# Kernel tuning notes

Hardware: AMD Instinct MI355X
Metric: run time of the kernel (lower is better)

## Reference

```python
import jax, jax.numpy as jnp
import numpy as np

N_ENT = 100000
N_REL = 500
IN_DIM = 128
OUT_DIM = 128
N_TRIP = 250000
BN_EPS = 1e-5
LRELU_SLOPE = 0.01


def setup_inputs() -> dict:
    key = jax.random.key(0)
    ks = jax.random.split(key, 10)
    heads = jax.random.randint(ks[0], (N_TRIP, 1), 0, N_ENT, dtype=jnp.int32)
    tails = jax.random.randint(ks[1], (N_TRIP, 1), 0, N_ENT, dtype=jnp.int32)
    rels = jax.random.randint(ks[2], (N_TRIP, 1), 0, N_REL, dtype=jnp.int32)
    triplets = jnp.concatenate([heads, tails, rels], axis=1)
    embed_range = (6.0 + 2.0) / OUT_DIM  # (margin + epsilon) / out_dim
    ent_embed = jax.random.uniform(ks[3], (N_ENT, IN_DIM), jnp.float32, -embed_range, embed_range)
    rel_embed = jax.random.uniform(ks[4], (N_REL, IN_DIM), jnp.float32, -embed_range, embed_range)
    a_w = jax.random.normal(ks[5], (OUT_DIM, 3 * IN_DIM), jnp.float32) * (1.414 * (2.0 / (3 * IN_DIM + OUT_DIM)) ** 0.5)
    a_b = jnp.zeros((OUT_DIM,), jnp.float32)
    a2_w = jax.random.normal(ks[6], (1, OUT_DIM), jnp.float32) * (1.414 * (2.0 / (OUT_DIM + 1)) ** 0.5)
    a2_b = jnp.zeros((1,), jnp.float32)
    return dict(
        triplets=triplets,
        ent_embed=ent_embed,
        rel_embed=rel_embed,
        a_w=a_w,
        a_b=a_b,
        a2_w=a2_w,
        a2_b=a2_b,
        bn0_g=jnp.ones((3 * IN_DIM,), jnp.float32),
        bn0_b=jnp.zeros((3 * IN_DIM,), jnp.float32),
        bn1_g=jnp.ones((OUT_DIM,), jnp.float32),
        bn1_b=jnp.zeros((OUT_DIM,), jnp.float32),
    )


def _batchnorm(x, gamma, beta):
    # training-mode BN: batch statistics over axis 0, biased variance
    mean = jnp.mean(x, axis=0)
    var = jnp.mean(jnp.square(x - mean), axis=0)
    return (x - mean) * jax.lax.rsqrt(var + BN_EPS) * gamma + beta


def _leaky_relu(x):
    return jnp.where(x >= 0, x, LRELU_SLOPE * x)


def reference(triplets, ent_embed, rel_embed, a_w, a_b, a2_w, a2_b,
              bn0_g, bn0_b, bn1_g, bn1_b):
    t0, t1, t2 = triplets[:, 0], triplets[:, 1], triplets[:, 2]
    e0 = ent_embed[t0]           # [n, in_dim]
    e1 = ent_embed[t1]           # [n, in_dim]
    r = rel_embed[t2]            # [n, in_dim]
    h_fwd = jnp.concatenate([e0, e1, r], axis=1)    # [n, 3*in_dim]
    h_bwd = jnp.concatenate([e1, e0, -r], axis=1)   # [n, 3*in_dim]
    h = jnp.concatenate([h_fwd, h_bwd], axis=0)     # [2n, 3*in_dim]
    h = _batchnorm(h, bn0_g, bn0_b)                 # dropout omitted (eval)
    c = _batchnorm(h @ a_w.T + a_b, bn1_g, bn1_b)   # [2n, out_dim]
    b = -_leaky_relu(c @ a2_w.T + a2_b)             # [2n, 1]
    e_b = jnp.exp(b)                                # [2n, 1]

    # edges[0] = cat(t0, t1); scatter-add messages into source node slots
    seg = jnp.concatenate([t0, t1], axis=0)         # [2n]
    temp1 = e_b * c                                 # [2n, out_dim]
    ebs = jax.ops.segment_sum(e_b, seg, num_segments=N_ENT)    # [N, 1]
    hs = jax.ops.segment_sum(temp1, seg, num_segments=N_ENT)   # [N, out_dim]
    ebs = jnp.where(ebs == 0, 1e-12, ebs)
    h_ent = hs / ebs                                # [N, out_dim]

    # scatter-mean of forward-direction messages by relation id
    rel_sum = jax.ops.segment_sum(temp1[:N_TRIP], t2, num_segments=N_REL)
    rel_cnt = jax.ops.segment_sum(jnp.ones((N_TRIP, 1), temp1.dtype), t2, num_segments=N_REL)
    h_rel = rel_sum / jnp.maximum(rel_cnt, 1.0)     # [R, out_dim]
    return h_ent, h_rel
```

## Files before the change

### kernel.cpp

```cpp
#include <hip/hip_runtime.h>
#include <hip/hip_bf16.h>

#define NE 100000
#define NR 500
#define DD 128
#define NT 250000
#define NEV 500000
#define RELOFF 12800000
#define TWO_NF 500000.0f
#define NTF 250000.0f
#define TBH 2048
#define NBH ((NT + TBH - 1)/TBH)
#define NBS ((NE + 1023)/1024)

typedef __attribute__((ext_vector_type(8))) short short8;
typedef __attribute__((ext_vector_type(4))) float f32x4;

__device__ __forceinline__ float bf2f(unsigned short u){
  unsigned int x = ((unsigned int)u) << 16;
  return __uint_as_float(x);
}
__device__ __forceinline__ float bf2f_lo(unsigned int u){ return __uint_as_float(u << 16); }
__device__ __forceinline__ float bf2f_hi(unsigned int u){ return __uint_as_float(u & 0xFFFF0000u); }
__device__ __forceinline__ unsigned short f2bf(float f){
  __hip_bfloat16 h = __float2bfloat16(f);
  return *reinterpret_cast<unsigned short*>(&h);
}
__device__ __forceinline__ void atomAddF(float* p, float v){ unsafeAtomicAdd(p, v); }
__device__ __forceinline__ float wredsum(float x){
  x += __shfl_xor(x, 1, 64);  x += __shfl_xor(x, 2, 64);  x += __shfl_xor(x, 4, 64);
  x += __shfl_xor(x, 8, 64);  x += __shfl_xor(x, 16, 64); x += __shfl_xor(x, 32, 64);
  return x;
}

__global__ __launch_bounds__(256) void k_hist(const int* __restrict__ trip,
                                              int* __restrict__ cnt, int* __restrict__ gHist){
  __shared__ int h[NR];
  int t = threadIdx.x;
  for (int r = t; r < NR; r += 256) h[r] = 0;
  __syncthreads();
  int b0 = blockIdx.x*TBH, b1 = min(b0+TBH, NT);
  for (int i = b0 + t; i < b1; i += 256){
    int t0 = trip[3*i], t1 = trip[3*i+1], t2 = trip[3*i+2];
    atomicAdd(&cnt[t0], 1);
    atomicAdd(&cnt[t1], 1);
    atomicAdd(&h[t2], 1);
  }
  __syncthreads();
  for (int r = t; r < NR; r += 256) gHist[blockIdx.x*NR + r] = h[r];
}

__global__ __launch_bounds__(512) void k_histscan(const int* __restrict__ gHist,
                                                  int* __restrict__ base, int* __restrict__ cntR,
                                                  int* __restrict__ offR){
  __shared__ int sm[512];
  int r = threadIdx.x;
  int s = 0;
  if (r < NR){
    for (int b = 0; b < NBH; ++b){ base[b*NR + r] = s; s += gHist[b*NR + r]; }
    cntR[r] = s;
  }
  sm[r] = (r < NR) ? s : 0;
  __syncthreads();
  for (int st = 1; st < 512; st <<= 1){
    int x = (r >= st) ? sm[r-st] : 0;
    __syncthreads();
    sm[r] += x;
    __syncthreads();
  }
  if (r < NR){
    int off = sm[r] - s;
    offR[r] = off;
    for (int b = 0; b < NBH; ++b) base[b*NR + r] += off;
  }
  if (r == 0) offR[NR] = NT;
}

__global__ __launch_bounds__(1024) void k_scan1(const int* __restrict__ cnt,
                                                int* __restrict__ off, int* __restrict__ bsum){
  __shared__ int wsum[16];
  int t = threadIdx.x, lane = t & 63, w = t >> 6;
  int i = blockIdx.x*1024 + t;
  int v = (i < NE) ? cnt[i] : 0;
  int x = v;
  #pragma unroll
  for (int s = 1; s < 64; s <<= 1){ int y = __shfl_up(x, s, 64); if (lane >= s) x += y; }
  if (lane == 63) wsum[w] = x;
  __syncthreads();
  if (w == 0 && lane < 16){
    int xs = wsum[lane];
    #pragma unroll
    for (int s = 1; s < 16; s <<= 1){ int y = __shfl_up(xs, s, 16); if ((lane & 15) >= s) xs += y; }
    wsum[lane] = xs;
  }
  __syncthreads();
  int wprev = (w == 0) ? 0 : wsum[w-1];
  int incl = wprev + x;
  if (i < NE) off[i] = incl - v;
  if (t == 1023) bsum[blockIdx.x] = incl;
}

__global__ __launch_bounds__(128) void k_scan2(const int* __restrict__ bsum,
                                               int* __restrict__ bbase, int* __restrict__ off){
  __shared__ int sm[128];
  int t = threadIdx.x;
  int v = (t < NBS) ? bsum[t] : 0;
  sm[t] = v; __syncthreads();
  for (int s = 1; s < 128; s <<= 1){
    int x = (t >= s) ? sm[t-s] : 0;
    __syncthreads();
    sm[t] += x;
    __syncthreads();
  }
  int incl = sm[t];
  if (t < NBS) bbase[t] = incl - v;
  if (t == NBS-1) off[NE] = incl;
}

__global__ __launch_bounds__(1024) void k_scan3(int* __restrict__ off, int* __restrict__ cur,
                                                const int* __restrict__ bbase){
  int i = blockIdx.x*1024 + threadIdx.x;
  if (i < NE){
    int o = off[i] + bbase[blockIdx.x];
    off[i] = o;
    cur[i] = o;
  }
}

__global__ void k_scat_ent(const int* __restrict__ trip, int* __restrict__ curE,
                           unsigned long long* __restrict__ evE){
  int i = blockIdx.x*blockDim.x + threadIdx.x;
  if (i < NT){
    int t0 = trip[3*i+0], t1 = trip[3*i+1], t2 = trip[3*i+2];
    int p0 = atomicAdd(&curE[t0], 1);
    unsigned long long e0 = (unsigned)t0 |
      ((unsigned long long)(((unsigned)t1 << 10) | ((unsigned)t2 << 1)) << 32);
    __builtin_nontemporal_store(e0, &evE[p0]);
    int p1 = atomicAdd(&curE[t1], 1);
    unsigned long long e1 = (unsigned)t1 |
      ((unsigned long long)(((unsigned)t0 << 10) | ((unsigned)t2 << 1) | 1u) << 32);
    __builtin_nontemporal_store(e1, &evE[p1]);
  }
}

__global__ __launch_bounds__(256) void k_scat_rel(const int* __restrict__ trip,
                                                  const int* __restrict__ base,
                                                  unsigned long long* __restrict__ evR){
  __shared__ int cur[NR];
  int t = threadIdx.x;
  for (int r = t; r < NR; r += 256) cur[r] = base[blockIdx.x*NR + r];
  __syncthreads();
  int b0 = blockIdx.x*TBH, b1 = min(b0+TBH, NT);
  for (int i = b0 + t; i < b1; i += 256){
    int t0 = trip[3*i], t1 = trip[3*i+1], t2 = trip[3*i+2];
    int p = atomicAdd(&cur[t2], 1);
    unsigned long long e = (unsigned)t0 | ((unsigned long long)(unsigned)t1 << 32);
    __builtin_nontemporal_store(e, &evR[p]);
  }
}

__global__ __launch_bounds__(256) void k_entstats(const float* __restrict__ ent, const int* __restrict__ cnt,
                                                  float* __restrict__ S, float* __restrict__ Q,
                                                  unsigned short* __restrict__ Xbf){
  int j = threadIdx.x & 127;
  int half = threadIdx.x >> 7;
  int r0 = blockIdx.x*128 + half;
  int r1 = min(blockIdx.x*128 + 128, NE);
  float s = 0.f, q = 0.f;
  for (int r = r0; r < r1; r += 2){
    float x = ent[(size_t)r*DD + j];
    Xbf[(size_t)r*DD + j] = f2bf(x);
    int w = cnt[r];
    if (w){
      float wf = (float)w;
      s += wf*x; q += wf*x*x;
    }
  }
  __shared__ float ss[256], qq[256];
  ss[threadIdx.x] = s; qq[threadIdx.x] = q; __syncthreads();
  if (half == 0){
    atomAddF(&S[j], ss[j] + ss[j+128]);
    atomAddF(&Q[j], qq[j] + qq[j+128]);
  }
}

__global__ void k_alpha(const float* __restrict__ rel, const int* __restrict__ cntR,
                        const float* __restrict__ S, const float* __restrict__ Q,
                        const float* __restrict__ bn0g, const float* __restrict__ bn0b,
                        float* __restrict__ alpha0, float* __restrict__ alpha1, float* __restrict__ alpha2,
                        float* __restrict__ beta0, float* __restrict__ beta1){
  int j = threadIdx.x;
  float qr = 0.f;
  for (int k = 0; k < NR; ++k){
    float w = (float)cntR[k];
    float x = rel[k*DD + j];
    qr += w*x*x;
  }
  float mean = S[j] / TWO_NF;
  float var  = Q[j] / TWO_NF - mean*mean;
  float inv  = rsqrtf(var + 1e-5f);
  float a0 = inv * bn0g[j];
  float a1 = inv * bn0g[128+j];
  alpha0[j] = a0; alpha1[j] = a1;
  beta0[j] = bn0b[j]     - mean*a0;
  beta1[j] = bn0b[128+j] - mean*a1;
  float varR = qr / NTF;
  alpha2[j] = rsqrtf(varR + 1e-5f) * bn0g[256+j];
}

__global__ void k_bias(const float* __restrict__ aw, const float* __restrict__ ab,
                       const float* __restrict__ bn0b,
                       const float* __restrict__ beta0, const float* __restrict__ beta1,
                       float* __restrict__ bias){
  int o = blockIdx.x, j = threadIdx.x;
  const float* r = aw + (size_t)o*384;
  float p = r[j]*beta0[j] + r[128+j]*beta1[j] + r[256+j]*bn0b[256+j];
  __shared__ float sm[128];
  sm[j] = p; __syncthreads();
  for (int s = 64; s > 0; s >>= 1){ if (j < s) sm[j] += sm[j+s]; __syncthreads(); }
  if (j == 0) bias[o] = ab[o] + sm[0];
}

__global__ void k_v(const float* __restrict__ rel, const float* __restrict__ aw,
                    const float* __restrict__ alpha2, float* __restrict__ V){
  int k = blockIdx.x, o = threadIdx.x;
  __shared__ float rl[128];
  rl[o] = rel[k*DD + o] * alpha2[o];
  __syncthreads();
  float acc = 0.f;
  #pragma unroll 8
  for (int j = 0; j < 128; ++j) acc += aw[(size_t)o*384 + 256 + j] * rl[j];
  V[k*DD + o] = acc;
}

__global__ void k_wfold2(const float* __restrict__ aw, const float* __restrict__ alpha0,
                         const float* __restrict__ alpha1, unsigned short* __restrict__ Wt2){
  int o = blockIdx.x;
  int k = threadIdx.x;
  float w;
  if (o < 128) w = aw[(size_t)o*384 + k] * alpha0[k];
  else         w = aw[(size_t)(o-128)*384 + 128 + k] * alpha1[k];
  Wt2[(size_t)o*128 + k] = f2bf(w);
}

__global__ __launch_bounds__(256) void k_u2(const unsigned short* __restrict__ Xbf,
                                            const unsigned short* __restrict__ Wt2,
                                            unsigned short* __restrict__ Uo){
  int tid = threadIdx.x;
  int w = tid >> 6, l = tid & 63;
  int col = l & 15, grp = l >> 4, kof = grp*8;
  int e0 = blockIdx.x*64;
  int ot0 = w*4;

  const unsigned short* wb0 = Wt2 + (size_t)((ot0+0)*16 + col)*128 + kof;
  const unsigned short* wb1 = Wt2 + (size_t)((ot0+1)*16 + col)*128 + kof;
  const unsigned short* wb2 = Wt2 + (size_t)((ot0+2)*16 + col)*128 + kof;
  const unsigned short* wb3 = Wt2 + (size_t)((ot0+3)*16 + col)*128 + kof;
  short8 b00 = *(const short8*)(wb0);
  short8 b01 = *(const short8*)(wb0+32);
  short8 b02 = *(const short8*)(wb0+64);
  short8 b03 = *(const short8*)(wb0+96);
  short8 b10 = *(const short8*)(wb1);
  short8 b11 = *(const short8*)(wb1+32);
  short8 b12 = *(const short8*)(wb1+64);
  short8 b13 = *(const short8*)(wb1+96);
  short8 b20 = *(const short8*)(wb2);
  short8 b21 = *(const short8*)(wb2+32);
  short8 b22 = *(const short8*)(wb2+64);
  short8 b23 = *(const short8*)(wb2+96);
  short8 b30 = *(const short8*)(wb3);
  short8 b31 = *(const short8*)(wb3+32);
  short8 b32 = *(const short8*)(wb3+64);
  short8 b33 = *(const short8*)(wb3+96);

  #pragma unroll
  for (int et = 0; et < 4; ++et){
    int ebase = e0 + et*16;
    int e = min(ebase + col, NE-1);
    const unsigned short* xrow = Xbf + (size_t)e*DD;
    short8 a0 = *(const short8*)(xrow + kof);
    short8 a1 = *(const short8*)(xrow + 32 + kof);
    short8 a2 = *(const short8*)(xrow + 64 + kof);
    short8 a3 = *(const short8*)(xrow + 96 + kof);
    f32x4 c0 = (f32x4){0.f,0.f,0.f,0.f};
    f32x4 c1 = (f32x4){0.f,0.f,0.f,0.f};
    f32x4 c2 = (f32x4){0.f,0.f,0.f,0.f};
    f32x4 c3 = (f32x4){0.f,0.f,0.f,0.f};
    c0 = __builtin_amdgcn_mfma_f32_16x16x32_bf16(a0, b00, c0, 0, 0, 0);
    c1 = __builtin_amdgcn_mfma_f32_16x16x32_bf16(a0, b10, c1, 0, 0, 0);
    c2 = __builtin_amdgcn_mfma_f32_16x16x32_bf16(a0, b20, c2, 0, 0, 0);
    c3 = __builtin_amdgcn_mfma_f32_16x16x32_bf16(a0, b30, c3, 0, 0, 0);
    c0 = __builtin_amdgcn_mfma_f32_16x16x32_bf16(a1, b01, c0, 0, 0, 0);
    c1 = __builtin_amdgcn_mfma_f32_16x16x32_bf16(a1, b11, c1, 0, 0, 0);
    c2 = __builtin_amdgcn_mfma_f32_16x16x32_bf16(a1, b21, c2, 0, 0, 0);
    c3 = __builtin_amdgcn_mfma_f32_16x16x32_bf16(a1, b31, c3, 0, 0, 0);
    c0 = __builtin_amdgcn_mfma_f32_16x16x32_bf16(a2, b02, c0, 0, 0, 0);
    c1 = __builtin_amdgcn_mfma_f32_16x16x32_bf16(a2, b12, c1, 0, 0, 0);
    c2 = __builtin_amdgcn_mfma_f32_16x16x32_bf16(a2, b22, c2, 0, 0, 0);
    c3 = __builtin_amdgcn_mfma_f32_16x16x32_bf16(a2, b32, c3, 0, 0, 0);
    c0 = __builtin_amdgcn_mfma_f32_16x16x32_bf16(a3, b03, c0, 0, 0, 0);
    c1 = __builtin_amdgcn_mfma_f32_16x16x32_bf16(a3, b13, c1, 0, 0, 0);
    c2 = __builtin_amdgcn_mfma_f32_16x16x32_bf16(a3, b23, c2, 0, 0, 0);
    c3 = __builtin_amdgcn_mfma_f32_16x16x32_bf16(a3, b33, c3, 0, 0, 0);
    #pragma unroll
    for (int r = 0; r < 4; ++r){
      int row = ebase + 4*grp + r;
      if (row < NE){
        size_t rb = (size_t)row*256 + col;
        Uo[rb + (ot0+0)*16] = f2bf(c0[r]);
        Uo[rb + (ot0+1)*16] = f2bf(c1[r]);
        Uo[rb + (ot0+2)*16] = f2bf(c2[r]);
        Uo[rb + (ot0+3)*16] = f2bf(c3[r]);
      }
    }
  }
}

__global__ __launch_bounds__(256) void k_c1b(const uint2* __restrict__ evE,
                   const unsigned short* __restrict__ U, const float* __restrict__ V,
                   const float* __restrict__ bias,
                   float* __restrict__ colsum, float* __restrict__ colsumsq){
  int lane = threadIdx.x & 63;
  int w = threadIdx.x >> 6;
  int wv = blockIdx.x*4 + w;
  int nwv = gridDim.x*4;
  int per = (NEV + nwv - 1) / nwv;
  int st = wv*per, en = min(st + per, NEV);
  int c0 = 2*lane, c1 = c0+1;
  float b0 = bias[c0], b1 = bias[c1];
  const ushort2* Ub = (const ushort2*)U;
  const float2*  Vp = (const float2*)V;
  float s0=0.f, s1=0.f, q0=0.f, q1=0.f;
  for (int bs = st; bs < en; bs += 64){
    int n = min(64, en - bs);
    uint2 ev = (bs + lane < en) ? evE[bs + lane] : make_uint2(0u, 0u);
    int j = 0;
    for (; j + 4 <= n; j += 4){
      unsigned ow0 = __shfl(ev.x, j, 64),   pk0 = __shfl(ev.y, j, 64);
      unsigned ow1 = __shfl(ev.x, j+1, 64), pk1 = __shfl(ev.y, j+1, 64);
      unsigned ow2 = __shfl(ev.x, j+2, 64), pk2 = __shfl(ev.y, j+2, 64);
      unsigned ow3 = __shfl(ev.x, j+3, 64), pk3 = __shfl(ev.y, j+3, 64);
      ushort2 a0 = Ub[(size_t)ow0*128 + lane];
      ushort2 g0 = Ub[(size_t)(pk0 >> 10)*128 + 64 + lane];
      float2  v0 = Vp[((pk0 >> 1) & 0x1FF)*64 + lane];
      ushort2 a1 = Ub[(size_t)ow1*128 + lane];
      ushort2 g1 = Ub[(size_t)(pk1 >> 10)*128 + 64 + lane];
      float2  v1 = Vp[((pk1 >> 1) & 0x1FF)*64 + lane];
      ushort2 a2 = Ub[(size_t)ow2*128 + lane];
      ushort2 g2 = Ub[(size_t)(pk2 >> 10)*128 + 64 + lane];
      float2  v2 = Vp[((pk2 >> 1) & 0x1FF)*64 + lane];
      ushort2 a3 = Ub[(size_t)ow3*128 + lane];
      ushort2 g3 = Ub[(size_t)(pk3 >> 10)*128 + 64 + lane];
      float2  v3 = Vp[((pk3 >> 1) & 0x1FF)*64 + lane];
      float sg0 = (pk0 & 1) ? -1.f : 1.f;
      float sg1 = (pk1 & 1) ? -1.f : 1.f;
      float sg2 = (pk2 & 1) ? -1.f : 1.f;
      float sg3 = (pk3 & 1) ? -1.f : 1.f;
      float y00 = bf2f(a0.x) + bf2f(g0.x) + sg0*v0.x + b0;
      float y01 = bf2f(a0.y) + bf2f(g0.y) + sg0*v0.y + b1;
      float y10 = bf2f(a1.x) + bf2f(g1.x) + sg1*v1.x + b0;
      float y11 = bf2f(a1.y) + bf2f(g1.y) + sg1*v1.y + b1;
      float y20 = bf2f(a2.x) + bf2f(g2.x) + sg2*v2.x + b0;
      float y21 = bf2f(a2.y) + bf2f(g2.y) + sg2*v2.y + b1;
      float y30 = bf2f(a3.x) + bf2f(g3.x) + sg3*v3.x + b0;
      float y31 = bf2f(a3.y) + bf2f(g3.y) + sg3*v3.y + b1;
      s0 += y00 + y10 + y20 + y30;
      s1 += y01 + y11 + y21 + y31;
      q0 += y00*y00 + y10*y10 + y20*y20 + y30*y30;
      q1 += y01*y01 + y11*y11 + y21*y21 + y31*y31;
    }
    for (; j < n; ++j){
      unsigned ow0 = __shfl(ev.x, j, 64), pk0 = __shfl(ev.y, j, 64);
      ushort2 a0 = Ub[(size_t)ow0*128 + lane];
      ushort2 g0 = Ub[(size_t)(pk0 >> 10)*128 + 64 + lane];
      float2  v0 = Vp[((pk0 >> 1) & 0x1FF)*64 + lane];
      float sg0 = (pk0 & 1) ? -1.f : 1.f;
      float y00 = bf2f(a0.x) + bf2f(g0.x) + sg0*v0.x + b0;
      float y01 = bf2f(a0.y) + bf2f(g0.y) + sg0*v0.y + b1;
      s0 += y00;  q0 += y00*y00;
      s1 += y01;  q1 += y01*y01;
    }
  }
  __shared__ float sred[4][128], qred[4][128];
  sred[w][c0] = s0; sred[w][c1] = s1;
  qred[w][c0] = q0; qred[w][c1] = q1;
  __syncthreads();
  int t = threadIdx.x;
  if (t < 128){
    atomAddF(&colsum[t],   sred[0][t] + sred[1][t] + sred[2][t] + sred[3][t]);
    atomAddF(&colsumsq[t], qred[0][t] + qred[1][t] + qred[2][t] + qred[3][t]);
  }
}

__global__ void k_bn1fin(const float* __restrict__ colsum, const float* __restrict__ colsumsq,
                         const float* __restrict__ bn1g, const float* __restrict__ bn1b,
                         const float* __restrict__ a2w, const float* __restrict__ a2b,
                         const float* __restrict__ biasv,
                         float* __restrict__ A1, float* __restrict__ B1,
                         float* __restrict__ a2A, float* __restrict__ sbase){
  int j = threadIdx.x;
  float mean = colsum[j] / TWO_NF;
  float var  = colsumsq[j] / TWO_NF - mean*mean;
  float A = rsqrtf(var + 1e-5f) * bn1g[j];
  float B = bn1b[j] - mean*A;
  A1[j] = A; B1[j] = B;
  float w2 = a2w[j];
  float aA = w2*A;
  a2A[j] = aA;
  __shared__ float sm[128], sm2[128];
  sm[j] = w2*B; sm2[j] = biasv[j]*aA;
  __syncthreads();
  for (int s = 64; s > 0; s >>= 1){
    if (j < s){ sm[j] += sm[j+s]; sm2[j] += sm2[j+s]; }
    __syncthreads();
  }
  if (j == 0){
    float sb = a2b[0] + sm[0];
    sbase[0] = sb;
    sbase[1] = sb + sm2[0];
  }
}

__global__ __launch_bounds__(256) void k_sigma(const unsigned short* __restrict__ U,
                                               const float* __restrict__ a2A,
                                               float* __restrict__ sig){
  int lane = threadIdx.x & 63;
  int e = blockIdx.x*4 + (threadIdx.x>>6);
  if (e >= NE) return;
  const uint2* Ur = (const uint2*)U;
  uint2 r = Ur[(size_t)e*64 + lane];
  int c = (lane & 31)*4;
  float4 w = *(const float4*)&a2A[c];
  float p = bf2f_lo(r.x)*w.x + bf2f_hi(r.x)*w.y + bf2f_lo(r.y)*w.z + bf2f_hi(r.y)*w.w;
  p += __shfl_xor(p, 1, 64); p += __shfl_xor(p, 2, 64); p += __shfl_xor(p, 4, 64);
  p += __shfl_xor(p, 8, 64); p += __shfl_xor(p, 16, 64);
  if ((lane & 31) == 0) sig[2*e + (lane >> 5)] = p;
}

__global__ __launch_bounds__(256) void k_rho(const float* __restrict__ V,
                                             const float* __restrict__ a2A,
                                             float* __restrict__ rho){
  int lane = threadIdx.x & 63;
  int k = blockIdx.x*4 + (threadIdx.x>>6);
  if (k >= NR) return;
  const float2* Vp = (const float2*)V;
  float2 v = Vp[(size_t)k*64 + lane];
  int c0 = 2*lane;
  float p = v.x*a2A[c0] + v.y*a2A[c0+1];
  p = wredsum(p);
  if (lane == 0) rho[k] = p;
}

__global__ __launch_bounds__(256) void k_gent(const uint2* __restrict__ evE, const int* __restrict__ offE,
                   const unsigned short* __restrict__ U, const float* __restrict__ V,
                   const float* __restrict__ sig, const float* __restrict__ rho,
                   const float* __restrict__ bias,
                   const float* __restrict__ A1, const float* __restrict__ B1,
                   const float* __restrict__ sbase,
                   float* __restrict__ out){
  int lane = threadIdx.x & 63;
  int e = blockIdx.x*4 + (threadIdx.x>>6);
  if (e >= NE) return;
  int c0 = 2*lane, c1 = c0+1;
  const ushort2* Ub = (const ushort2*)U;
  const float2*  Vp = (const float2*)V;
  ushort2 u0 = Ub[(size_t)e*128 + lane];
  float base0 = bf2f(u0.x) + bias[c0], base1 = bf2f(u0.y) + bias[c1];
  float pb  = sbase[1];
  float s0e = sig[2*e];
  float accU0=0.f, accU1=0.f, accV0=0.f, accV1=0.f, sep=0.f;
  int p0 = offE[e], p1 = offE[e+1];
  for (int bs = p0; bs < p1; bs += 64){
    int n = min(64, p1 - bs);
    unsigned ev = 0u; float ebl = 0.f;
    if (bs + lane < p1){
      ev = evE[bs + lane].y;
      int oth = ev >> 10, rl = (ev >> 1) & 0x1FF;
      float sg = (ev & 1) ? -1.f : 1.f;
      float s = s0e + sig[2*oth + 1] + sg*rho[rl] + pb;
      float bb = (s >= 0.f) ? -s : -0.01f*s;
      ebl = expf(bb);
    }
    sep += ebl;
    int j = 0;
    for (; j + 4 <= n; j += 4){
      unsigned e0 = __shfl(ev, j, 64);
      unsigned e1 = __shfl(ev, j+1, 64);
      unsigned e2 = __shfl(ev, j+2, 64);
      unsigned e3 = __shfl(ev, j+3, 64);
      float eb0 = __shfl(ebl, j, 64);
      float eb1 = __shfl(ebl, j+1, 64);
      float eb2 = __shfl(ebl, j+2, 64);
      float eb3 = __shfl(ebl, j+3, 64);
      ushort2 g0 = Ub[(size_t)(e0 >> 10)*128 + 64 + lane];
      ushort2 g1 = Ub[(size_t)(e1 >> 10)*128 + 64 + lane];
      ushort2 g2 = Ub[(size_t)(e2 >> 10)*128 + 64 + lane];
      ushort2 g3 = Ub[(size_t)(e3 >> 10)*128 + 64 + lane];
      float2 v0 = Vp[((e0 >> 1) & 0x1FF)*64 + lane];
      float2 v1 = Vp[((e1 >> 1) & 0x1FF)*64 + lane];
      float2 v2 = Vp[((e2 >> 1) & 0x1FF)*64 + lane];
      float2 v3 = Vp[((e3 >> 1) & 0x1FF)*64 + lane];
      float w0 = (e0 & 1) ? -eb0 : eb0;
      float w1 = (e1 & 1) ? -eb1 : eb1;
      float w2 = (e2 & 1) ? -eb2 : eb2;
      float w3 = (e3 & 1) ? -eb3 : eb3;
      accU0 += eb0*bf2f(g0.x); accU1 += eb0*bf2f(g0.y);
      accV0 += w0*v0.x;        accV1 += w0*v0.y;
      accU0 += eb1*bf2f(g1.x); accU1 += eb1*bf2f(g1.y);
      accV0 += w1*v1.x;        accV1 += w1*v1.y;
      accU0 += eb2*bf2f(g2.x); accU1 += eb2*bf2f(g2.y);
      accV0 += w2*v2.x;        accV1 += w2*v2.y;
      accU0 += eb3*bf2f(g3.x); accU1 += eb3*bf2f(g3.y);
      accV0 += w3*v3.x;        accV1 += w3*v3.y;
    }
    for (; j < n; ++j){
      unsigned e0 = __shfl(ev, j, 64);
      float eb0 = __shfl(ebl, j, 64);
      ushort2 g0 = Ub[(size_t)(e0 >> 10)*128 + 64 + lane];
      float2 v0 = Vp[((e0 >> 1) & 0x1FF)*64 + lane];
      float w0 = (e0 & 1) ? -eb0 : eb0;
      accU0 += eb0*bf2f(g0.x); accU1 += eb0*bf2f(g0.y);
      accV0 += w0*v0.x;        accV1 += w0*v0.y;
    }
  }
  float se = wredsum(sep);
  float sY0 = se*base0 + accU0 + accV0;
  float sY1 = se*base1 + accU1 + accV1;
  float hs0 = A1[c0]*sY0 + B1[c0]*se;
  float hs1 = A1[c1]*sY1 + B1[c1]*se;
  float d = (se == 0.f) ? 1e-12f : se;
  out[(size_t)e*DD + c0] = hs0/d;
  out[(size_t)e*DD + c1] = hs1/d;
}

__global__ __launch_bounds__(256) void k_grel(const uint2* __restrict__ evR, const int* __restrict__ offR,
                   const unsigned short* __restrict__ U, const float* __restrict__ V,
                   const float* __restrict__ sig, const float* __restrict__ rho,
                   const float* __restrict__ bias,
                   const float* __restrict__ A1, const float* __restrict__ B1,
                   const float* __restrict__ sbase,
                   float* __restrict__ out){
  int lane = threadIdx.x & 63;
  int k = blockIdx.x >> 3;
  int wvs = (blockIdx.x & 7)*4 + (threadIdx.x >> 6);
  int c0 = 2*lane, c1 = c0+1;
  const ushort2* Ub = (const ushort2*)U;
  const float2*  Vp = (const float2*)V;
  float2 v = Vp[(size_t)k*64 + lane];
  float vb0 = v.x + bias[c0], vb1 = v.y + bias[c1];
  float rpb = rho[k] + sbase[1];
  float accY0=0.f, accY1=0.f, sep=0.f;
  int p0 = offR[k], p1 = offR[k+1];
  int tot = p1 - p0, per = (tot + 31) >> 5;
  int st = p0 + wvs*per, en = min(st + per, p1);
  for (int bs = st; bs < en; bs += 64){
    int n = min(64, en - bs);
    uint2 ev = make_uint2(0u, 0u); float ebl = 0.f;
    if (bs + lane < en){
      ev = evR[bs + lane];
      float s = sig[2*ev.x] + sig[2*ev.y + 1] + rpb;
      float bb = (s >= 0.f) ? -s : -0.01f*s;
      ebl = expf(bb);
    }
    sep += ebl;
    int j = 0;
    for (; j + 2 <= n; j += 2){
      unsigned a0 = __shfl(ev.x, j, 64),   d0 = __shfl(ev.y, j, 64);
      unsigned a1 = __shfl(ev.x, j+1, 64), d1 = __shfl(ev.y, j+1, 64);
      float eb0 = __shfl(ebl, j, 64);
      float eb1 = __shfl(ebl, j+1, 64);
      ushort2 ua0 = Ub[(size_t)a0*128 + lane];
      ushort2 ud0 = Ub[(size_t)d0*128 + 64 + lane];
      ushort2 ua1 = Ub[(size_t)a1*128 + lane];
      ushort2 ud1 = Ub[(size_t)d1*128 + 64 + lane];
      accY0 += eb0*(bf2f(ua0.x) + bf2f(ud0.x));
      accY1 += eb0*(bf2f(ua0.y) + bf2f(ud0.y));
      accY0 += eb1*(bf2f(ua1.x) + bf2f(ud1.x));
      accY1 += eb1*(bf2f(ua1.y) + bf2f(ud1.y));
    }
    for (; j < n; ++j){
      unsigned a0 = __shfl(ev.x, j, 64), d0 = __shfl(ev.y, j, 64);
      float eb0 = __shfl(ebl, j, 64);
      ushort2 ua0 = Ub[(size_t)a0*128 + lane];
      ushort2 ud0 = Ub[(size_t)d0*128 + 64 + lane];
      accY0 += eb0*(bf2f(ua0.x) + bf2f(ud0.x));
      accY1 += eb0*(bf2f(ua0.y) + bf2f(ud0.y));
    }
  }
  float se = wredsum(sep);
  float sY0 = accY0 + se*vb0;
  float sY1 = accY1 + se*vb1;
  float r0 = A1[c0]*sY0 + B1[c0]*se;
  float r1 = A1[c1]*sY1 + B1[c1]*se;
  atomAddF(&out[(size_t)RELOFF + (size_t)k*DD + c0], r0);
  atomAddF(&out[(size_t)RELOFF + (size_t)k*DD + c1], r1);
}

__global__ void k_fin_rel(float* __restrict__ out, const int* __restrict__ cntR){
  int idx = blockIdx.x*blockDim.x + threadIdx.x;
  int k = idx >> 7;
  float c = fmaxf((float)cntR[k], 1.f);
  out[RELOFF + idx] = out[RELOFF + idx] / c;
}

extern "C" void kernel_launch(void* const* d_in, const int* in_sizes, int n_in,
                              void* d_out, int out_size, void* d_ws, size_t ws_size,
                              hipStream_t stream) {
  (void)in_sizes; (void)n_in; (void)ws_size; (void)out_size;
  const int*   trip = (const int*)  d_in[0];
  const float* ent  = (const float*)d_in[1];
  const float* rel  = (const float*)d_in[2];
  const float* aw   = (const float*)d_in[3];
  const float* ab   = (const float*)d_in[4];
  const float* a2w  = (const float*)d_in[5];
  const float* a2b  = (const float*)d_in[6];
  const float* bn0g = (const float*)d_in[7];
  const float* bn0b = (const float*)d_in[8];
  const float* bn1g = (const float*)d_in[9];
  const float* bn1b = (const float*)d_in[10];
  float* out = (float*)d_out;
  unsigned short* Xbf = (unsigned short*)d_out;

  char* w = (char*)d_ws;
  size_t off = 0;
  auto take = [&](size_t bytes) -> char* {
    char* p = w + off;
    off = (off + bytes + 511) & ~(size_t)511;
    return p;
  };
  float* S        = (float*)take(512);
  float* Q        = (float*)take(512);
  float* colsum   = (float*)take(512);
  float* colsumsq = (float*)take(512);
  int*   cnt      = (int*)  take((size_t)NE*4);
  size_t zero_end = off;
  int*   cntR   = (int*)  take((size_t)NR*4);
  float* alpha0 = (float*)take(512);
  float* alpha1 = (float*)take(512);
  float* alpha2 = (float*)take(512);
  float* beta0  = (float*)take(512);
  float* beta1  = (float*)take(512);
  float* biasv  = (float*)take(512);
  float* A1     = (float*)take(512);
  float* B1     = (float*)take(512);
  float* a2A    = (float*)take(512);
  float* sbase  = (float*)take(512);
  float* rho    = (float*)take((size_t)NR*4);
  float* sig    = (float*)take((size_t)NE*2*4);
  int*   offE   = (int*)  take((size_t)(NE+1)*4);
  int*   curE   = (int*)  take((size_t)NE*4);
  int*   offR   = (int*)  take((size_t)(NR+1)*4);
  int*   gHist  = (int*)  take((size_t)NBH*NR*4);
  int*   gBase  = (int*)  take((size_t)NBH*NR*4);
  int*   bsum   = (int*)  take((size_t)NBS*4);
  int*   bbase  = (int*)  take((size_t)NBS*4);
  unsigned long long* evE = (unsigned long long*)take((size_t)NEV*8);
  unsigned long long* evR = (unsigned long long*)take((size_t)NT*8);
  float* V      = (float*)take((size_t)NR*DD*4);
  unsigned short* Wt2 = (unsigned short*)take((size_t)256*128*2);
  unsigned short* U   = (unsigned short*)take((size_t)NE*256*2);

  hipMemsetAsync((char*)d_out + (size_t)RELOFF*4, 0, (size_t)NR*DD*4, stream);
  hipMemsetAsync(d_ws, 0, zero_end, stream);

  k_hist     <<<NBH, 256, 0, stream>>>(trip, cnt, gHist);
  k_histscan <<<1, 512, 0, stream>>>(gHist, gBase, cntR, offR);
  k_scan1    <<<NBS, 1024, 0, stream>>>(cnt, offE, bsum);
  k_scan2    <<<1, 128, 0, stream>>>(bsum, bbase, offE);
  k_scan3    <<<NBS, 1024, 0, stream>>>(offE, curE, bbase);
  k_scat_ent <<<(NT+255)/256, 256, 0, stream>>>(trip, curE, evE);
  k_scat_rel <<<NBH, 256, 0, stream>>>(trip, gBase, evR);
  k_entstats <<<(NE+127)/128, 256, 0, stream>>>(ent, cnt, S, Q, Xbf);
  k_alpha    <<<1, 128, 0, stream>>>(rel, cntR, S, Q, bn0g, bn0b, alpha0, alpha1, alpha2, beta0, beta1);
  k_bias     <<<128, 128, 0, stream>>>(aw, ab, bn0b, beta0, beta1, biasv);
  k_v        <<<NR, 128, 0, stream>>>(rel, aw, alpha2, V);
  k_wfold2   <<<256, 128, 0, stream>>>(aw, alpha0, alpha1, Wt2);
  k_u2       <<<1563, 256, 0, stream>>>(Xbf, Wt2, U);
  k_c1b      <<<2048, 256, 0, stream>>>((const uint2*)evE, U, V, biasv, colsum, colsumsq);
  k_bn1fin   <<<1, 128, 0, stream>>>(colsum, colsumsq, bn1g, bn1b, a2w, a2b, biasv, A1, B1, a2A, sbase);
  k_sigma    <<<NE/4, 256, 0, stream>>>(U, a2A, sig);
  k_rho      <<<(NR+3)/4, 256, 0, stream>>>(V, a2A, rho);
  k_gent     <<<NE/4, 256, 0, stream>>>((const uint2*)evE, offE, U, V, sig, rho, biasv, A1, B1, sbase, out);
  k_grel     <<<NR*8, 256, 0, stream>>>((const uint2*)evR, offR, U, V, sig, rho, biasv, A1, B1, sbase, out);
  k_fin_rel  <<<(NR*DD)/256, 256, 0, stream>>>(out, cntR);
}
```

Before: 375.9 us.

## Merge small launches, use bf16 relation vectors in gathers, reduce relation output in-block

```diff
diff --git a/kernel.cpp b/kernel.cpp
--- a/kernel.cpp
+++ b/kernel.cpp
@@ -32,6 +32,11 @@
   x += __shfl_xor(x, 8, 64);  x += __shfl_xor(x, 16, 64); x += __shfl_xor(x, 32, 64);
   return x;
 }
+__device__ __forceinline__ int wredsumi(int x){
+  x += __shfl_xor(x, 1, 64);  x += __shfl_xor(x, 2, 64);  x += __shfl_xor(x, 4, 64);
+  x += __shfl_xor(x, 8, 64);  x += __shfl_xor(x, 16, 64); x += __shfl_xor(x, 32, 64);
+  return x;
+}
 
 __global__ __launch_bounds__(256) void k_hist(const int* __restrict__ trip,
                                               int* __restrict__ cnt, int* __restrict__ gHist){
@@ -100,31 +105,25 @@
   if (t == 1023) bsum[blockIdx.x] = incl;
 }
 
-__global__ __launch_bounds__(128) void k_scan2(const int* __restrict__ bsum,
-                                               int* __restrict__ bbase, int* __restrict__ off){
-  __shared__ int sm[128];
+__global__ __launch_bounds__(1024) void k_scan23(const int* __restrict__ bsum,
+                                                 int* __restrict__ off, int* __restrict__ cur){
+  __shared__ int basesh;
   int t = threadIdx.x;
-  int v = (t < NBS) ? bsum[t] : 0;
-  sm[t] = v; __syncthreads();
-  for (int s = 1; s < 128; s <<= 1){
-    int x = (t >= s) ? sm[t-s] : 0;
-    __syncthreads();
-    sm[t] += x;
-    __syncthreads();
-  }
-  int incl = sm[t];
-  if (t < NBS) bbase[t] = incl - v;
-  if (t == NBS-1) off[NE] = incl;
-}
-
-__global__ __launch_bounds__(1024) void k_scan3(int* __restrict__ off, int* __restrict__ cur,
-                                                const int* __restrict__ bbase){
-  int i = blockIdx.x*1024 + threadIdx.x;
+  if (t < 64){
+    int acc = 0;
+    for (int b = t; b < blockIdx.x; b += 64) acc += bsum[b];
+    acc = wredsumi(acc);
+    if (t == 0) basesh = acc;
+  }
+  __syncthreads();
+  int base = basesh;
+  int i = blockIdx.x*1024 + t;
   if (i < NE){
-    int o = off[i] + bbase[blockIdx.x];
+    int o = off[i] + base;
     off[i] = o;
     cur[i] = o;
   }
+  if (blockIdx.x == NBS-1 && t == 0) off[NE] = base + bsum[NBS-1];
 }
 
 __global__ void k_scat_ent(const int* __restrict__ trip, int* __restrict__ curE,
@@ -208,39 +207,39 @@
   alpha2[j] = rsqrtf(varR + 1e-5f) * bn0g[256+j];
 }
 
-__global__ void k_bias(const float* __restrict__ aw, const float* __restrict__ ab,
-                       const float* __restrict__ bn0b,
-                       const float* __restrict__ beta0, const float* __restrict__ beta1,
-                       float* __restrict__ bias){
-  int o = blockIdx.x, j = threadIdx.x;
-  const float* r = aw + (size_t)o*384;
-  float p = r[j]*beta0[j] + r[128+j]*beta1[j] + r[256+j]*bn0b[256+j];
+__global__ __launch_bounds__(128) void k_fold(const float* __restrict__ aw, const float* __restrict__ ab,
+                        const float* __restrict__ bn0b, const float* __restrict__ rel,
+                        const float* __restrict__ alpha0, const float* __restrict__ alpha1,
+                        const float* __restrict__ alpha2,
+                        const float* __restrict__ beta0, const float* __restrict__ beta1,
+                        float* __restrict__ bias, float* __restrict__ V,
+                        unsigned short* __restrict__ Vbf, unsigned short* __restrict__ Wt2){
   __shared__ float sm[128];
-  sm[j] = p; __syncthreads();
-  for (int s = 64; s > 0; s >>= 1){ if (j < s) sm[j] += sm[j+s]; __syncthreads(); }
-  if (j == 0) bias[o] = ab[o] + sm[0];
-}
-
-__global__ void k_v(const float* __restrict__ rel, const float* __restrict__ aw,
-                    const float* __restrict__ alpha2, float* __restrict__ V){
-  int k = blockIdx.x, o = threadIdx.x;
-  __shared__ float rl[128];
-  rl[o] = rel[k*DD + o] * alpha2[o];
-  __syncthreads();
-  float acc = 0.f;
-  #pragma unroll 8
-  for (int j = 0; j < 128; ++j) acc += aw[(size_t)o*384 + 256 + j] * rl[j];
-  V[k*DD + o] = acc;
-}
-
-__global__ void k_wfold2(const float* __restrict__ aw, const float* __restrict__ alpha0,
-                         const float* __restrict__ alpha1, unsigned short* __restrict__ Wt2){
-  int o = blockIdx.x;
-  int k = threadIdx.x;
-  float w;
-  if (o < 128) w = aw[(size_t)o*384 + k] * alpha0[k];
-  else         w = aw[(size_t)(o-128)*384 + 128 + k] * alpha1[k];
-  Wt2[(size_t)o*128 + k] = f2bf(w);
+  int b = blockIdx.x, j = threadIdx.x;
+  if (b < 128){
+    int o = b;
+    const float* r = aw + (size_t)o*384;
+    float p = r[j]*beta0[j] + r[128+j]*beta1[j] + r[256+j]*bn0b[256+j];
+    sm[j] = p; __syncthreads();
+    for (int s = 64; s > 0; s >>= 1){ if (j < s) sm[j] += sm[j+s]; __syncthreads(); }
+    if (j == 0) bias[o] = ab[o] + sm[0];
+  } else if (b < 628){
+    int k = b - 128;
+    sm[j] = rel[k*DD + j] * alpha2[j];
+    __syncthreads();
+    float acc = 0.f;
+    #pragma unroll 8
+    for (int q = 0; q < 128; ++q) acc += aw[(size_t)j*384 + 256 + q] * sm[q];
+    V[k*DD + j] = acc;
+    Vbf[k*DD + j] = f2bf(acc);
+  } else {
+    int o = b - 628;
+    int k = j;
+    float w;
+    if (o < 128) w = aw[(size_t)o*384 + k] * alpha0[k];
+    else         w = aw[(size_t)(o-128)*384 + 128 + k] * alpha1[k];
+    Wt2[(size_t)o*128 + k] = f2bf(w);
+  }
 }
 
 __global__ __launch_bounds__(256) void k_u2(const unsigned short* __restrict__ Xbf,
@@ -317,7 +316,7 @@
 }
 
 __global__ __launch_bounds__(256) void k_c1b(const uint2* __restrict__ evE,
-                   const unsigned short* __restrict__ U, const float* __restrict__ V,
+                   const unsigned short* __restrict__ U, const unsigned short* __restrict__ Vbf,
                    const float* __restrict__ bias,
                    float* __restrict__ colsum, float* __restrict__ colsumsq){
   int lane = threadIdx.x & 63;
@@ -329,7 +328,7 @@
   int c0 = 2*lane, c1 = c0+1;
   float b0 = bias[c0], b1 = bias[c1];
   const ushort2* Ub = (const ushort2*)U;
-  const float2*  Vp = (const float2*)V;
+  const ushort2* Vb = (const ushort2*)Vbf;
   float s0=0.f, s1=0.f, q0=0.f, q1=0.f;
   for (int bs = st; bs < en; bs += 64){
     int n = min(64, en - bs);
@@ -342,28 +341,28 @@
       unsigned ow3 = __shfl(ev.x, j+3, 64), pk3 = __shfl(ev.y, j+3, 64);
       ushort2 a0 = Ub[(size_t)ow0*128 + lane];
       ushort2 g0 = Ub[(size_t)(pk0 >> 10)*128 + 64 + lane];
-      float2  v0 = Vp[((pk0 >> 1) & 0x1FF)*64 + lane];
+      ushort2 v0 = Vb[((pk0 >> 1) & 0x1FF)*64 + lane];
       ushort2 a1 = Ub[(size_t)ow1*128 + lane];
       ushort2 g1 = Ub[(size_t)(pk1 >> 10)*128 + 64 + lane];
-      float2  v1 = Vp[((pk1 >> 1) & 0x1FF)*64 + lane];
+      ushort2 v1 = Vb[((pk1 >> 1) & 0x1FF)*64 + lane];
       ushort2 a2 = Ub[(size_t)ow2*128 + lane];
       ushort2 g2 = Ub[(size_t)(pk2 >> 10)*128 + 64 + lane];
-      float2  v2 = Vp[((pk2 >> 1) & 0x1FF)*64 + lane];
+      ushort2 v2 = Vb[((pk2 >> 1) & 0x1FF)*64 + lane];
       ushort2 a3 = Ub[(size_t)ow3*128 + lane];
       ushort2 g3 = Ub[(size_t)(pk3 >> 10)*128 + 64 + lane];
-      float2  v3 = Vp[((pk3 >> 1) & 0x1FF)*64 + lane];
+      ushort2 v3 = Vb[((pk3 >> 1) & 0x1FF)*64 + lane];
       float sg0 = (pk0 & 1) ? -1.f : 1.f;
       float sg1 = (pk1 & 1) ? -1.f : 1.f;
       float sg2 = (pk2 & 1) ? -1.f : 1.f;
       float sg3 = (pk3 & 1) ? -1.f : 1.f;
-      float y00 = bf2f(a0.x) + bf2f(g0.x) + sg0*v0.x + b0;
-      float y01 = bf2f(a0.y) + bf2f(g0.y) + sg0*v0.y + b1;
-      float y10 = bf2f(a1.x) + bf2f(g1.x) + sg1*v1.x + b0;
-      float y11 = bf2f(a1.y) + bf2f(g1.y) + sg1*v1.y + b1;
-      float y20 = bf2f(a2.x) + bf2f(g2.x) + sg2*v2.x + b0;
-      float y21 = bf2f(a2.y) + bf2f(g2.y) + sg2*v2.y + b1;
-      float y30 = bf2f(a3.x) + bf2f(g3.x) + sg3*v3.x + b0;
-      float y31 = bf2f(a3.y) + bf2f(g3.y) + sg3*v3.y + b1;
+      float y00 = bf2f(a0.x) + bf2f(g0.x) + sg0*bf2f(v0.x) + b0;
+      float y01 = bf2f(a0.y) + bf2f(g0.y) + sg0*bf2f(v0.y) + b1;
+      float y10 = bf2f(a1.x) + bf2f(g1.x) + sg1*bf2f(v1.x) + b0;
+      float y11 = bf2f(a1.y) + bf2f(g1.y) + sg1*bf2f(v1.y) + b1;
+      float y20 = bf2f(a2.x) + bf2f(g2.x) + sg2*bf2f(v2.x) + b0;
+      float y21 = bf2f(a2.y) + bf2f(g2.y) + sg2*bf2f(v2.y) + b1;
+      float y30 = bf2f(a3.x) + bf2f(g3.x) + sg3*bf2f(v3.x) + b0;
+      float y31 = bf2f(a3.y) + bf2f(g3.y) + sg3*bf2f(v3.y) + b1;
       s0 += y00 + y10 + y20 + y30;
       s1 += y01 + y11 + y21 + y31;
       q0 += y00*y00 + y10*y10 + y20*y20 + y30*y30;
@@ -373,10 +372,10 @@
       unsigned ow0 = __shfl(ev.x, j, 64), pk0 = __shfl(ev.y, j, 64);
       ushort2 a0 = Ub[(size_t)ow0*128 + lane];
       ushort2 g0 = Ub[(size_t)(pk0 >> 10)*128 + 64 + lane];
-      float2  v0 = Vp[((pk0 >> 1) & 0x1FF)*64 + lane];
+      ushort2 v0 = Vb[((pk0 >> 1) & 0x1FF)*64 + lane];
       float sg0 = (pk0 & 1) ? -1.f : 1.f;
-      float y00 = bf2f(a0.x) + bf2f(g0.x) + sg0*v0.x + b0;
-      float y01 = bf2f(a0.y) + bf2f(g0.y) + sg0*v0.y + b1;
+      float y00 = bf2f(a0.x) + bf2f(g0.x) + sg0*bf2f(v0.x) + b0;
+      float y01 = bf2f(a0.y) + bf2f(g0.y) + sg0*bf2f(v0.y) + b1;
       s0 += y00;  q0 += y00*y00;
       s1 += y01;  q1 += y01*y01;
     }
@@ -421,38 +420,35 @@
   }
 }
 
-__global__ __launch_bounds__(256) void k_sigma(const unsigned short* __restrict__ U,
-                                               const float* __restrict__ a2A,
-                                               float* __restrict__ sig){
+__global__ __launch_bounds__(256) void k_sigrho(const unsigned short* __restrict__ U,
+                                                const float* __restrict__ V,
+                                                const float* __restrict__ a2A,
+                                                float* __restrict__ sig, float* __restrict__ rho){
   int lane = threadIdx.x & 63;
-  int e = blockIdx.x*4 + (threadIdx.x>>6);
-  if (e >= NE) return;
-  const uint2* Ur = (const uint2*)U;
-  uint2 r = Ur[(size_t)e*64 + lane];
-  int c = (lane & 31)*4;
-  float4 w = *(const float4*)&a2A[c];
-  float p = bf2f_lo(r.x)*w.x + bf2f_hi(r.x)*w.y + bf2f_lo(r.y)*w.z + bf2f_hi(r.y)*w.w;
-  p += __shfl_xor(p, 1, 64); p += __shfl_xor(p, 2, 64); p += __shfl_xor(p, 4, 64);
-  p += __shfl_xor(p, 8, 64); p += __shfl_xor(p, 16, 64);
-  if ((lane & 31) == 0) sig[2*e + (lane >> 5)] = p;
-}
-
-__global__ __launch_bounds__(256) void k_rho(const float* __restrict__ V,
-                                             const float* __restrict__ a2A,
-                                             float* __restrict__ rho){
-  int lane = threadIdx.x & 63;
-  int k = blockIdx.x*4 + (threadIdx.x>>6);
-  if (k >= NR) return;
-  const float2* Vp = (const float2*)V;
-  float2 v = Vp[(size_t)k*64 + lane];
-  int c0 = 2*lane;
-  float p = v.x*a2A[c0] + v.y*a2A[c0+1];
-  p = wredsum(p);
-  if (lane == 0) rho[k] = p;
+  if (blockIdx.x < NE/4){
+    int e = blockIdx.x*4 + (threadIdx.x>>6);
+    const uint2* Ur = (const uint2*)U;
+    uint2 r = Ur[(size_t)e*64 + lane];
+    int c = (lane & 31)*4;
+    float4 w = *(const float4*)&a2A[c];
+    float p = bf2f_lo(r.x)*w.x + bf2f_hi(r.x)*w.y + bf2f_lo(r.y)*w.z + bf2f_hi(r.y)*w.w;
+    p += __shfl_xor(p, 1, 64); p += __shfl_xor(p, 2, 64); p += __shfl_xor(p, 4, 64);
+    p += __shfl_xor(p, 8, 64); p += __shfl_xor(p, 16, 64);
+    if ((lane & 31) == 0) sig[2*e + (lane >> 5)] = p;
+  } else {
+    int k = (blockIdx.x - NE/4)*4 + (threadIdx.x>>6);
+    if (k >= NR) return;
+    const float2* Vp = (const float2*)V;
+    float2 v = Vp[(size_t)k*64 + lane];
+    int c0 = 2*lane;
+    float p = v.x*a2A[c0] + v.y*a2A[c0+1];
+    p = wredsum(p);
+    if (lane == 0) rho[k] = p;
+  }
 }
 
 __global__ __launch_bounds__(256) void k_gent(const uint2* __restrict__ evE, const int* __restrict__ offE,
-                   const unsigned short* __restrict__ U, const float* __restrict__ V,
+                   const unsigned short* __restrict__ U, const unsigned short* __restrict__ Vbf,
                    const float* __restrict__ sig, const float* __restrict__ rho,
                    const float* __restrict__ bias,
                    const float* __restrict__ A1, const float* __restrict__ B1,
@@ -463,7 +459,7 @@
   if (e >= NE) return;
   int c0 = 2*lane, c1 = c0+1;
   const ushort2* Ub = (const ushort2*)U;
-  const float2*  Vp = (const float2*)V;
+  const ushort2* Vb = (const ushort2*)Vbf;
   ushort2 u0 = Ub[(size_t)e*128 + lane];
   float base0 = bf2f(u0.x) + bias[c0], base1 = bf2f(u0.y) + bias[c1];
   float pb  = sbase[1];
@@ -496,31 +492,31 @@
       ushort2 g1 = Ub[(size_t)(e1 >> 10)*128 + 64 + lane];
       ushort2 g2 = Ub[(size_t)(e2 >> 10)*128 + 64 + lane];
       ushort2 g3 = Ub[(size_t)(e3 >> 10)*128 + 64 + lane];
-      float2 v0 = Vp[((e0 >> 1) & 0x1FF)*64 + lane];
-      float2 v1 = Vp[((e1 >> 1) & 0x1FF)*64 + lane];
-      float2 v2 = Vp[((e2 >> 1) & 0x1FF)*64 + lane];
-      float2 v3 = Vp[((e3 >> 1) & 0x1FF)*64 + lane];
+      ushort2 v0 = Vb[((e0 >> 1) & 0x1FF)*64 + lane];
+      ushort2 v1 = Vb[((e1 >> 1) & 0x1FF)*64 + lane];
+      ushort2 v2 = Vb[((e2 >> 1) & 0x1FF)*64 + lane];
+      ushort2 v3 = Vb[((e3 >> 1) & 0x1FF)*64 + lane];
       float w0 = (e0 & 1) ? -eb0 : eb0;
       float w1 = (e1 & 1) ? -eb1 : eb1;
       float w2 = (e2 & 1) ? -eb2 : eb2;
       float w3 = (e3 & 1) ? -eb3 : eb3;
       accU0 += eb0*bf2f(g0.x); accU1 += eb0*bf2f(g0.y);
-      accV0 += w0*v0.x;        accV1 += w0*v0.y;
+      accV0 += w0*bf2f(v0.x);  accV1 += w0*bf2f(v0.y);
       accU0 += eb1*bf2f(g1.x); accU1 += eb1*bf2f(g1.y);
-      accV0 += w1*v1.x;        accV1 += w1*v1.y;
+      accV0 += w1*bf2f(v1.x);  accV1 += w1*bf2f(v1.y);
       accU0 += eb2*bf2f(g2.x); accU1 += eb2*bf2f(g2.y);
-      accV0 += w2*v2.x;        accV1 += w2*v2.y;
+      accV0 += w2*bf2f(v2.x);  accV1 += w2*bf2f(v2.y);
       accU0 += eb3*bf2f(g3.x); accU1 += eb3*bf2f(g3.y);
-      accV0 += w3*v3.x;        accV1 += w3*v3.y;
+      accV0 += w3*bf2f(v3.x);  accV1 += w3*bf2f(v3.y);
     }
     for (; j < n; ++j){
       unsigned e0 = __shfl(ev, j, 64);
       float eb0 = __shfl(ebl, j, 64);
       ushort2 g0 = Ub[(size_t)(e0 >> 10)*128 + 64 + lane];
-      float2 v0 = Vp[((e0 >> 1) & 0x1FF)*64 + lane];
+      ushort2 v0 = Vb[((e0 >> 1) & 0x1FF)*64 + lane];
       float w0 = (e0 & 1) ? -eb0 : eb0;
       accU0 += eb0*bf2f(g0.x); accU1 += eb0*bf2f(g0.y);
-      accV0 += w0*v0.x;        accV1 += w0*v0.y;
+      accV0 += w0*bf2f(v0.x);  accV1 += w0*bf2f(v0.y);
     }
   }
   float se = wredsum(sep);
@@ -533,16 +529,17 @@
   out[(size_t)e*DD + c1] = hs1/d;
 }
 
-__global__ __launch_bounds__(256) void k_grel(const uint2* __restrict__ evR, const int* __restrict__ offR,
+__global__ __launch_bounds__(1024) void k_grel2(const uint2* __restrict__ evR, const int* __restrict__ offR,
                    const unsigned short* __restrict__ U, const float* __restrict__ V,
                    const float* __restrict__ sig, const float* __restrict__ rho,
                    const float* __restrict__ bias,
                    const float* __restrict__ A1, const float* __restrict__ B1,
-                   const float* __restrict__ sbase,
+                   const float* __restrict__ sbase, const int* __restrict__ cntR,
                    float* __restrict__ out){
+  __shared__ float rA[16][64], rB[16][64], sepw[16];
   int lane = threadIdx.x & 63;
-  int k = blockIdx.x >> 3;
-  int wvs = (blockIdx.x & 7)*4 + (threadIdx.x >> 6);
+  int w = threadIdx.x >> 6;
+  int k = blockIdx.x;
   int c0 = 2*lane, c1 = c0+1;
   const ushort2* Ub = (const ushort2*)U;
   const float2*  Vp = (const float2*)V;
@@ -551,12 +548,10 @@
   float rpb = rho[k] + sbase[1];
   float accY0=0.f, accY1=0.f, sep=0.f;
   int p0 = offR[k], p1 = offR[k+1];
-  int tot = p1 - p0, per = (tot + 31) >> 5;
-  int st = p0 + wvs*per, en = min(st + per, p1);
-  for (int bs = st; bs < en; bs += 64){
-    int n = min(64, en - bs);
+  for (int bs = p0 + w*64; bs < p1; bs += 16*64){
+    int n = min(64, p1 - bs);
     uint2 ev = make_uint2(0u, 0u); float ebl = 0.f;
-    if (bs + lane < en){
+    if (bs + lane < p1){
       ev = evR[bs + lane];
       float s = sig[2*ev.x] + sig[2*ev.y + 1] + rpb;
       float bb = (s >= 0.f) ? -s : -0.01f*s;
@@ -587,20 +582,24 @@
       accY1 += eb0*(bf2f(ua0.y) + bf2f(ud0.y));
     }
   }
-  float se = wredsum(sep);
-  float sY0 = accY0 + se*vb0;
-  float sY1 = accY1 + se*vb1;
-  float r0 = A1[c0]*sY0 + B1[c0]*se;
-  float r1 = A1[c1]*sY1 + B1[c1]*se;
-  atomAddF(&out[(size_t)RELOFF + (size_t)k*DD + c0], r0);
-  atomAddF(&out[(size_t)RELOFF + (size_t)k*DD + c1], r1);
-}
-
-__global__ void k_fin_rel(float* __restrict__ out, const int* __restrict__ cntR){
-  int idx = blockIdx.x*blockDim.x + threadIdx.x;
-  int k = idx >> 7;
-  float c = fmaxf((float)cntR[k], 1.f);
-  out[RELOFF + idx] = out[RELOFF + idx] / c;
+  float se_w = wredsum(sep);
+  rA[w][lane] = accY0;
+  rB[w][lane] = accY1;
+  if (lane == 0) sepw[w] = se_w;
+  __syncthreads();
+  if (threadIdx.x < 64){
+    int l = threadIdx.x;
+    float sY0 = 0.f, sY1 = 0.f, se = 0.f;
+    #pragma unroll
+    for (int ww = 0; ww < 16; ++ww){ sY0 += rA[ww][l]; sY1 += rB[ww][l]; se += sepw[ww]; }
+    sY0 += se*vb0;
+    sY1 += se*vb1;
+    float r0 = A1[c0]*sY0 + B1[c0]*se;
+    float r1 = A1[c1]*sY1 + B1[c1]*se;
+    float cdiv = fmaxf((float)cntR[k], 1.f);
+    out[(size_t)RELOFF + (size_t)k*DD + c0] = r0/cdiv;
+    out[(size_t)RELOFF + (size_t)k*DD + c1] = r1/cdiv;
+  }
 }
 
 extern "C" void kernel_launch(void* const* d_in, const int* in_sizes, int n_in,
@@ -653,34 +652,29 @@
   int*   gHist  = (int*)  take((size_t)NBH*NR*4);
   int*   gBase  = (int*)  take((size_t)NBH*NR*4);
   int*   bsum   = (int*)  take((size_t)NBS*4);
-  int*   bbase  = (int*)  take((size_t)NBS*4);
   unsigned long long* evE = (unsigned long long*)take((size_t)NEV*8);
   unsigned long long* evR = (unsigned long long*)take((size_t)NT*8);
   float* V      = (float*)take((size_t)NR*DD*4);
+  unsigned short* Vbf = (unsigned short*)take((size_t)NR*DD*2);
   unsigned short* Wt2 = (unsigned short*)take((size_t)256*128*2);
   unsigned short* U   = (unsigned short*)take((size_t)NE*256*2);
 
-  hipMemsetAsync((char*)d_out + (size_t)RELOFF*4, 0, (size_t)NR*DD*4, stream);
   hipMemsetAsync(d_ws, 0, zero_end, stream);
 
   k_hist     <<<NBH, 256, 0, stream>>>(trip, cnt, gHist);
   k_histscan <<<1, 512, 0, stream>>>(gHist, gBase, cntR, offR);
   k_scan1    <<<NBS, 1024, 0, stream>>>(cnt, offE, bsum);
-  k_scan2    <<<1, 128, 0, stream>>>(bsum, bbase, offE);
-  k_scan3    <<<NBS, 1024, 0, stream>>>(offE, curE, bbase);
+  k_scan23   <<<NBS, 1024, 0, stream>>>(bsum, offE, curE);
   k_scat_ent <<<(NT+255)/256, 256, 0, stream>>>(trip, curE, evE);
   k_scat_rel <<<NBH, 256, 0, stream>>>(trip, gBase, evR);
   k_entstats <<<(NE+127)/128, 256, 0, stream>>>(ent, cnt, S, Q, Xbf);
   k_alpha    <<<1, 128, 0, stream>>>(rel, cntR, S, Q, bn0g, bn0b, alpha0, alpha1, alpha2, beta0, beta1);
-  k_bias     <<<128, 128, 0, stream>>>(aw, ab, bn0b, beta0, beta1, biasv);
-  k_v        <<<NR, 128, 0, stream>>>(rel, aw, alpha2, V);
-  k_wfold2   <<<256, 128, 0, stream>>>(aw, alpha0, alpha1, Wt2);
+  k_fold     <<<884, 128, 0, stream>>>(aw, ab, bn0b, rel, alpha0, alpha1, alpha2, beta0, beta1,
+                                       biasv, V, Vbf, Wt2);
   k_u2       <<<1563, 256, 0, stream>>>(Xbf, Wt2, U);
-  k_c1b      <<<2048, 256, 0, stream>>>((const uint2*)evE, U, V, biasv, colsum, colsumsq);
+  k_c1b      <<<2048, 256, 0, stream>>>((const uint2*)evE, U, Vbf, biasv, colsum, colsumsq);
   k_bn1fin   <<<1, 128, 0, stream>>>(colsum, colsumsq, bn1g, bn1b, a2w, a2b, biasv, A1, B1, a2A, sbase);
-  k_sigma    <<<NE/4, 256, 0, stream>>>(U, a2A, sig);
-  k_rho      <<<(NR+3)/4, 256, 0, stream>>>(V, a2A, rho);
-  k_gent     <<<NE/4, 256, 0, stream>>>((const uint2*)evE, offE, U, V, sig, rho, biasv, A1, B1, sbase, out);
-  k_grel     <<<NR*8, 256, 0, stream>>>((const uint2*)evR, offR, U, V, sig, rho, biasv, A1, B1, sbase, out);
-  k_fin_rel  <<<(NR*DD)/256, 256, 0, stream>>>(out, cntR);
-}
+  k_sigrho   <<<NE/4 + (NR+3)/4, 256, 0, stream>>>(U, V, a2A, sig, rho);
+  k_gent     <<<NE/4, 256, 0, stream>>>((const uint2*)evE, offE, U, Vbf, sig, rho, biasv, A1, B1, sbase, out);
+  k_grel2    <<<NR, 1024, 0, stream>>>((const uint2*)evR, offR, U, V, sig, rho, biasv, A1, B1, sbase, cntR, out);
+}
```

After: 348.9 us (median of 2 runs). 7.2% less time.
